# Kernel optimization log

Hardware: AMD Instinct MI355X
Metric: run time of the kernel (lower is better)

The kernel has to match this reference:

```python
import jax, jax.numpy as jnp
import numpy as np

N = 50000
E = 800000
IN_DIM = 128
HID = 32
HEADS = 8
OUT_DIM = 64
BN_EPS = 1e-5
NEG_SLOPE = 0.2


def batch_norm(x, gamma, beta, mean, var):
    # eval-mode BatchNorm1d using running statistics
    return (x - mean) * jax.lax.rsqrt(var + BN_EPS) * gamma + beta


def gat_conv(x, src, dst, W, att_src, att_dst, heads, out_ch, n):
    """PyG GATConv (shared src/dst lin), self-loops already included in src/dst.
    x: [n, in]; W: [in, heads*out_ch]; att_*: [heads, out_ch].
    Returns [n, heads, out_ch]."""
    h = (x @ W).reshape(n, heads, out_ch)                       # node features per head
    a_s = jnp.einsum('nho,ho->nh', h, att_src)                  # [n, heads]
    a_d = jnp.einsum('nho,ho->nh', h, att_dst)
    e = jax.nn.leaky_relu(a_s[src] + a_d[dst], NEG_SLOPE)       # [e, heads]
    # segment softmax over incoming edges of each dst node
    mx = jax.ops.segment_max(e, dst, num_segments=n)
    ex = jnp.exp(e - mx[dst])
    denom = jax.ops.segment_sum(ex, dst, num_segments=n)
    alpha = ex / (denom[dst] + 1e-16)                           # [e, heads]
    out = jax.ops.segment_sum(alpha[:, :, None] * h[src], dst, num_segments=n)
    return out                                                  # [n, heads, out_ch]


def setup_inputs() -> dict:
    key = jax.random.key(0)
    ks = jax.random.split(key, 24)
    inp = {}
    inp['x'] = jax.random.normal(ks[0], (N, IN_DIM), dtype=jnp.float32)
    inp['edge_index'] = jax.random.randint(ks[1], (2, E), 0, N, dtype=jnp.int64)
    s = 0.05
    inp['W1'] = jax.random.normal(ks[2], (IN_DIM, HEADS * HID), dtype=jnp.float32) * s
    inp['a_src1'] = jax.random.normal(ks[3], (HEADS, HID), dtype=jnp.float32) * s
    inp['a_dst1'] = jax.random.normal(ks[4], (HEADS, HID), dtype=jnp.float32) * s
    inp['b1'] = jnp.zeros((HEADS * HID,), dtype=jnp.float32)
    inp['W2'] = jax.random.normal(ks[5], (HEADS * HID, OUT_DIM), dtype=jnp.float32) * s
    inp['a_src2'] = jax.random.normal(ks[6], (1, OUT_DIM), dtype=jnp.float32) * s
    inp['a_dst2'] = jax.random.normal(ks[7], (1, OUT_DIM), dtype=jnp.float32) * s
    inp['b2'] = jnp.zeros((OUT_DIM,), dtype=jnp.float32)
    # projection Linear(out_dim -> in_dim)
    inp['Wp'] = jax.random.normal(ks[8], (OUT_DIM, IN_DIM), dtype=jnp.float32) * s
    inp['bp'] = jnp.zeros((IN_DIM,), dtype=jnp.float32)
    # BatchNorm params (eval mode running stats)
    for i, d in [(1, HEADS * HID), (2, OUT_DIM), (3, IN_DIM)]:
        k0, k1, k2, k3 = jax.random.split(ks[8 + i], 4)
        inp[f'g{i}'] = 1.0 + 0.1 * jax.random.normal(k0, (d,), dtype=jnp.float32)
        inp[f'be{i}'] = 0.1 * jax.random.normal(k1, (d,), dtype=jnp.float32)
        inp[f'm{i}'] = 0.1 * jax.random.normal(k2, (d,), dtype=jnp.float32)
        inp[f'v{i}'] = jax.random.uniform(k3, (d,), dtype=jnp.float32, minval=0.5, maxval=1.5)
    return inp


def reference(x, edge_index, W1, a_src1, a_dst1, b1, W2, a_src2, a_dst2, b2,
              Wp, bp, g1, be1, m1, v1, g2, be2, m2, v2, g3, be3, m3, v3):
    n = x.shape[0]
    loops = jnp.arange(n, dtype=edge_index.dtype)
    src = jnp.concatenate([edge_index[0], loops])   # add_self_loops=True (PyG default)
    dst = jnp.concatenate([edge_index[1], loops])

    h = gat_conv(x, src, dst, W1, a_src1, a_dst1, HEADS, HID, n)
    h = h.reshape(n, HEADS * HID) + b1              # concat=True
    h = jax.nn.elu(batch_norm(h, g1, be1, m1, v1))  # dropout is no-op in eval

    h = gat_conv(h, src, dst, W2, a_src2, a_dst2, 1, OUT_DIM, n)
    h = h.reshape(n, OUT_DIM) + b2                  # concat=False, heads=1 -> mean == identity
    h = jax.nn.elu(batch_norm(h, g2, be2, m2, v2))

    h = h @ Wp + bp
    return batch_norm(h, g3, be3, m3, v3)
```

## Files before the change

kernel.cpp:

```cpp
#include <hip/hip_runtime.h>
#include <math.h>

#define NEG_SLOPE 0.2f
#define BN_EPS 1e-5f

typedef __bf16 bf16x8 __attribute__((ext_vector_type(8)));
typedef float  f32x4  __attribute__((ext_vector_type(4)));

__device__ __forceinline__ float elu_f(float x){ return x > 0.f ? x : expm1f(x); }
__device__ __forceinline__ float lrelu_f(float x){ return x > 0.f ? x : NEG_SLOPE * x; }

__device__ __forceinline__ float b2f(ushort u){
    union { uint i; float f; } v; v.i = (uint)u << 16; return v.f;
}
__device__ __forceinline__ ushort f2b(float f){
    union { float f; uint i; } v; v.f = f;
    uint r = v.i + 0x7FFFu + ((v.i >> 16) & 1u);
    return (ushort)(r >> 16);
}

__global__ void setup_kernel(const void* ei, int n_check, long long N, int* flag64,
    const float* __restrict__ W1, const float* __restrict__ W2, const float* __restrict__ Wp,
    ushort* __restrict__ wt1, ushort* __restrict__ wt2, ushort* __restrict__ wtp,
    const float* b1, const float* b2, const float* bp,
    const float* g1, const float* be1, const float* m1, const float* v1,
    const float* g2, const float* be2, const float* m2, const float* v2,
    const float* g3, const float* be3, const float* m3, const float* v3,
    float* par)
{
    int b = blockIdx.x, t = threadIdx.x;
    if (b == 0) {
        __shared__ int oks;
        if (t == 0) oks = 1;
        __syncthreads();
        const long long* p = (const long long*)ei;
        int ok = 1;
        for (int i = t; i < n_check; i += 256) {
            long long v = p[i];
            if (v < 0 || v >= N) ok = 0;
        }
        if (!ok) oks = 0;
        __syncthreads();
        if (t == 0) *flag64 = oks;
        { float s = g1[t] * rsqrtf(v1[t] + BN_EPS); par[t] = s;        par[256 + t] = b1[t] * s + be1[t] - m1[t] * s; }
        if (t < 64)  { float s = g2[t] * rsqrtf(v2[t] + BN_EPS); par[512 + t] = s;  par[576 + t] = b2[t] * s + be2[t] - m2[t] * s; }
        if (t < 128) { float s = g3[t] * rsqrtf(v3[t] + BN_EPS); par[640 + t] = s;  par[768 + t] = bp[t] * s + be3[t] - m3[t] * s; }
    } else {
        int idx = (b - 1) * 256 + t;
        if (idx < 32768) {
            int n = idx >> 7, k = idx & 127;
            wt1[idx] = f2b(W1[k * 256 + n]);
        } else if (idx < 49152) {
            int j = idx - 32768;
            int n = j >> 8, k = j & 255;
            wt2[j] = f2b(W2[k * 64 + n]);
        } else if (idx < 57344) {
            int j = idx - 49152;
            int n = j >> 6, k = j & 63;
            wtp[j] = f2b(Wp[k * 128 + n]);
        }
    }
}

__device__ __forceinline__ void get_edge(const void* ei, int e, int E, int f64, int& s, int& d)
{
    if (e < E) {
        if (f64) { const long long* p = (const long long*)ei; s = (int)p[e]; d = (int)p[E + e]; }
        else     { const int*       p = (const int*)ei;       s = p[e];      d = p[E + e]; }
    } else {
        s = d = e - E;
    }
}

__global__ void count_kernel(const void* ei, int E, int N, const int* flag64, int* deg)
{
    int i = blockIdx.x * blockDim.x + threadIdx.x;
    int ET = E + N;
    if (i >= ET) return;
    int s, d;
    get_edge(ei, i, E, *flag64, s, d);
    atomicAdd(&deg[d], 1);
}

__global__ void scan1_kernel(const int* __restrict__ deg, int N, int* __restrict__ bsum)
{
    int b = blockIdx.x, t = threadIdx.x;
    int base = b * 4096 + t * 16;
    int s = 0;
    #pragma unroll
    for (int k = 0; k < 16; k += 4) {
        int idx = base + k;
        if (idx + 3 < N) {
            int4 v = *reinterpret_cast<const int4*>(&deg[idx]);
            s += v.x + v.y + v.z + v.w;
        } else {
            for (int q = 0; q < 4; ++q) if (idx + q < N) s += deg[idx + q];
        }
    }
    #pragma unroll
    for (int off = 1; off < 64; off <<= 1) s += __shfl_xor(s, off);
    __shared__ int wsum[4];
    if ((t & 63) == 0) wsum[t >> 6] = s;
    __syncthreads();
    if (t == 0) bsum[b] = wsum[0] + wsum[1] + wsum[2] + wsum[3];
}

__global__ void scan2_kernel(const int* __restrict__ bsum, int nb, int* __restrict__ bpre)
{
    if (threadIdx.x == 0) {
        int r = 0;
        for (int i = 0; i < nb; ++i) { bpre[i] = r; r += bsum[i]; }
        bpre[nb] = r;
    }
}

__global__ void scan3_kernel(const int* __restrict__ deg, int N,
                             const int* __restrict__ bpre, int nb,
                             int* __restrict__ rowptr, int* __restrict__ fillptr)
{
    int b = blockIdx.x, t = threadIdx.x;
    int base = b * 4096 + t * 16;
    int loc[16];
    int s = 0;
    #pragma unroll
    for (int k = 0; k < 16; ++k) {
        int idx = base + k;
        int d = (idx < N) ? deg[idx] : 0;
        loc[k] = s; s += d;
    }
    int lane = t & 63;
    int incl = s;
    #pragma unroll
    for (int off = 1; off < 64; off <<= 1) {
        int v = __shfl_up(incl, off);
        if (lane >= off) incl += v;
    }
    __shared__ int wsum[4];
    if (lane == 63) wsum[t >> 6] = incl;
    __syncthreads();
    int woff = 0;
    int w = t >> 6;
    for (int i = 0; i < w; ++i) woff += wsum[i];
    int off0 = bpre[b] + woff + incl - s;
    #pragma unroll
    for (int k = 0; k < 16; ++k) {
        int idx = base + k;
        if (idx < N) { rowptr[idx] = off0 + loc[k]; fillptr[idx] = off0 + loc[k]; }
    }
    if (b == 0 && t == 0) rowptr[N] = bpre[nb];
}

__global__ void fill_kernel(const void* ei, int E, int N, const int* flag64,
                            int* fillptr, int* esrc)
{
    int i = blockIdx.x * blockDim.x + threadIdx.x;
    int ET = E + N;
    if (i >= ET) return;
    int s, d;
    get_edge(ei, i, E, *flag64, s, d);
    int pos = atomicAdd(&fillptr[d], 1);
    esrc[pos] = s;
}

template<int ATYPE, int OMODE, int ATT>
__global__ __launch_bounds__(256) void mgemm_kernel(const void* __restrict__ Ap,
    const ushort* __restrict__ Bt, void* __restrict__ Cp, int M, int K, int NC,
    const float* __restrict__ S, const float* __restrict__ Cc,
    const float* __restrict__ att_s, const float* __restrict__ att_d,
    float* __restrict__ as_out, float* __restrict__ ad_out)
{
    const int BM = 128, LDA = 72;
    __shared__ __align__(16) ushort As[BM][LDA];
    __shared__ __align__(16) ushort Bs[64][LDA];
    int t = threadIdx.x;
    int m0 = blockIdx.x * BM, n0 = blockIdx.y * 64;
    int w = t >> 6, l = t & 63;
    int wm = w >> 1, wn = w & 1;
    int r16 = l & 15, kg = l >> 4;

    f32x4 acc[4][2];
    #pragma unroll
    for (int mi = 0; mi < 4; ++mi)
        #pragma unroll
        for (int ni = 0; ni < 2; ++ni)
            acc[mi][ni] = (f32x4){0.f, 0.f, 0.f, 0.f};

    for (int kb = 0; kb < K; kb += 64) {
        if (ATYPE == 0) {
            const float* A = (const float*)Ap;
            #pragma unroll
            for (int p = 0; p < 8; ++p) {
                int r = (t >> 4) + p * 16, c4 = (t & 15) * 4;
                int gm = m0 + r;
                float4 v = (gm < M) ? *reinterpret_cast<const float4*>(&A[(size_t)gm * K + kb + c4])
                                    : make_float4(0.f, 0.f, 0.f, 0.f);
                ushort4 u; u.x = f2b(v.x); u.y = f2b(v.y); u.z = f2b(v.z); u.w = f2b(v.w);
                *reinterpret_cast<ushort4*>(&As[r][c4]) = u;
            }
        } else {
            const ushort* A = (const ushort*)Ap;
            #pragma unroll
            for (int p = 0; p < 4; ++p) {
                int r = (t >> 3) + p * 32, c8 = (t & 7) * 8;
                int gm = m0 + r;
                uint4 v = (gm < M) ? *reinterpret_cast<const uint4*>(&A[(size_t)gm * K + kb + c8])
                                   : make_uint4(0u, 0u, 0u, 0u);
                *reinterpret_cast<uint4*>(&As[r][c8]) = v;
            }
        }
        #pragma unroll
        for (int p = 0; p < 2; ++p) {
            int r = (t >> 3) + p * 32, c8 = (t & 7) * 8;
            uint4 v = *reinterpret_cast<const uint4*>(&Bt[(size_t)(n0 + r) * K + kb + c8]);
            *reinterpret_cast<uint4*>(&Bs[r][c8]) = v;
        }
        __syncthreads();
        #pragma unroll
        for (int kk = 0; kk < 2; ++kk) {
            bf16x8 bB[2], bA[4];
            #pragma unroll
            for (int ni = 0; ni < 2; ++ni)
                bB[ni] = *reinterpret_cast<const bf16x8*>(&Bs[wn * 32 + ni * 16 + r16][kk * 32 + kg * 8]);
            #pragma unroll
            for (int mi = 0; mi < 4; ++mi)
                bA[mi] = *reinterpret_cast<const bf16x8*>(&As[wm * 64 + mi * 16 + r16][kk * 32 + kg * 8]);
            #pragma unroll
            for (int mi = 0; mi < 4; ++mi)
                #pragma unroll
                for (int ni = 0; ni < 2; ++ni)
                    acc[mi][ni] = __builtin_amdgcn_mfma_f32_16x16x32_bf16(bA[mi], bB[ni], acc[mi][ni], 0, 0, 0);
        }
        __syncthreads();
    }
    #pragma unroll
    for (int mi = 0; mi < 4; ++mi) {
        #pragma unroll
        for (int ni = 0; ni < 2; ++ni) {
            #pragma unroll
            for (int rg = 0; rg < 4; ++rg) {
                int gm = m0 + wm * 64 + mi * 16 + kg * 4 + rg;
                int gc = n0 + wn * 32 + ni * 16 + r16;
                if (gm < M) {
                    float v = acc[mi][ni][rg];
                    if (OMODE == 0) ((ushort*)Cp)[(size_t)gm * NC + gc] = f2b(v);
                    else            ((float*)Cp)[(size_t)gm * NC + gc] = v * S[gc] + Cc[gc];
                }
            }
        }
    }
    if (ATT) {
        int head = (n0 >> 5) + wn;
        float cs0 = att_s[n0 + wn * 32 + r16], cs1 = att_s[n0 + wn * 32 + 16 + r16];
        float cd0 = att_d[n0 + wn * 32 + r16], cd1 = att_d[n0 + wn * 32 + 16 + r16];
        float sp[4][4], dp[4][4];
        #pragma unroll
        for (int mi = 0; mi < 4; ++mi)
            #pragma unroll
            for (int rg = 0; rg < 4; ++rg) {
                sp[mi][rg] = acc[mi][0][rg] * cs0 + acc[mi][1][rg] * cs1;
                dp[mi][rg] = acc[mi][0][rg] * cd0 + acc[mi][1][rg] * cd1;
            }
        #pragma unroll
        for (int off = 1; off < 16; off <<= 1)
            #pragma unroll
            for (int mi = 0; mi < 4; ++mi)
                #pragma unroll
                for (int rg = 0; rg < 4; ++rg) {
                    sp[mi][rg] += __shfl_xor(sp[mi][rg], off);
                    dp[mi][rg] += __shfl_xor(dp[mi][rg], off);
                }
        if (r16 == 0) {
            #pragma unroll
            for (int mi = 0; mi < 4; ++mi)
                #pragma unroll
                for (int rg = 0; rg < 4; ++rg) {
                    int gm = m0 + wm * 64 + mi * 16 + kg * 4 + rg;
                    if (gm < M) {
                        as_out[gm * 8 + head] = sp[mi][rg];
                        ad_out[gm * 8 + head] = dp[mi][rg];
                    }
                }
        }
    }
}

__global__ void att2_kernel(const ushort* __restrict__ h2,
                            const float* __restrict__ a_src, const float* __restrict__ a_dst,
                            float* __restrict__ as2, float* __restrict__ ad2, int N)
{
    int wid = (blockIdx.x * blockDim.x + threadIdx.x) >> 6;
    int lane = threadIdx.x & 63;
    if (wid >= N) return;
    float v = b2f(h2[(size_t)wid * 64 + lane]);
    float s = v * a_src[lane];
    float d = v * a_dst[lane];
    #pragma unroll
    for (int off = 32; off; off >>= 1) {
        s += __shfl_down(s, off, 64);
        d += __shfl_down(d, off, 64);
    }
    if (lane == 0) { as2[wid] = s; ad2[wid] = d; }
}

__global__ void wden1_kernel(const float* __restrict__ as1, const float* __restrict__ ad1,
                             const int* __restrict__ rowptr, const int* __restrict__ esrc,
                             float* __restrict__ walpha, int N)
{
    int wid = (blockIdx.x * blockDim.x + threadIdx.x) >> 6;
    int lane = threadIdx.x & 63;
    if (wid >= N) return;
    int h = lane & 7, j = lane >> 3;
    float ad = ad1[wid * 8 + h];
    int beg = rowptr[wid], end = rowptr[wid + 1];
    float den = 0.f;
    for (int i = beg + j; i < end; i += 8) {
        int src = esrc[i];
        float w = __expf(lrelu_f(as1[src * 8 + h] + ad));
        walpha[(size_t)i * 8 + h] = w;
        den += w;
    }
    den += __shfl_xor(den, 8);
    den += __shfl_xor(den, 16);
    den += __shfl_xor(den, 32);
    float inv = 1.f / (den + 1e-16f);
    for (int i = beg + j; i < end; i += 8)
        walpha[(size_t)i * 8 + h] *= inv;
}

__global__ void wden2_kernel(const float* __restrict__ as2, const float* __restrict__ ad2,
                             const int* __restrict__ rowptr, const int* __restrict__ esrc,
                             float* __restrict__ walpha, int N)
{
    int wid = (blockIdx.x * blockDim.x + threadIdx.x) >> 6;
    int lane = threadIdx.x & 63;
    if (wid >= N) return;
    float ad = ad2[wid];
    int beg = rowptr[wid], end = rowptr[wid + 1];
    float den = 0.f;
    for (int i = beg + lane; i < end; i += 64) {
        float w = __expf(lrelu_f(as2[esrc[i]] + ad));
        walpha[i] = w;
        den += w;
    }
    #pragma unroll
    for (int off = 1; off < 64; off <<= 1) den += __shfl_xor(den, off);
    float inv = 1.f / (den + 1e-16f);
    for (int i = beg + lane; i < end; i += 64)
        walpha[i] *= inv;
}

__global__ void agg1_kernel(const ushort* __restrict__ h1, const float* __restrict__ walpha,
                            const int* __restrict__ rowptr, const int* __restrict__ esrc,
                            const float* __restrict__ par,
                            ushort* __restrict__ outb, int N)
{
    int wid = (blockIdx.x * blockDim.x + threadIdx.x) >> 6;
    int lane = threadIdx.x & 63;
    if (wid >= N) return;
    int beg = rowptr[wid], end = rowptr[wid + 1];
    int li = lane & 31, half = lane >> 5;
    int hh = li >> 2;
    float acc[8] = {0.f, 0.f, 0.f, 0.f, 0.f, 0.f, 0.f, 0.f};

    auto edge1 = [&](int ii) {
        int src = esrc[ii];
        float al = walpha[(size_t)ii * 8 + hh];
        uint4 r = *reinterpret_cast<const uint4*>(&h1[(size_t)src * 256 + li * 8]);
        union { uint u; float f; } c0, c1;
        c0.u = r.x << 16; c1.u = r.x & 0xffff0000u; acc[0] += al * c0.f; acc[1] += al * c1.f;
        c0.u = r.y << 16; c1.u = r.y & 0xffff0000u; acc[2] += al * c0.f; acc[3] += al * c1.f;
        c0.u = r.z << 16; c1.u = r.z & 0xffff0000u; acc[4] += al * c0.f; acc[5] += al * c1.f;
        c0.u = r.w << 16; c1.u = r.w & 0xffff0000u; acc[6] += al * c0.f; acc[7] += al * c1.f;
    };
    int i = beg + half;
    for (; i + 6 < end; i += 8) { edge1(i); edge1(i + 2); edge1(i + 4); edge1(i + 6); }
    for (; i < end; i += 2) edge1(i);

    #pragma unroll
    for (int f = 0; f < 8; ++f) acc[f] += __shfl_xor(acc[f], 32, 64);
    if (half == 0) {
        int f0 = li * 8;
        const float* S1 = par;
        const float* C1 = par + 256;
        ushort o[8];
        #pragma unroll
        for (int f = 0; f < 8; ++f) o[f] = f2b(elu_f(acc[f] * S1[f0 + f] + C1[f0 + f]));
        uint4 pk;
        pk.x = (uint)o[0] | ((uint)o[1] << 16);
        pk.y = (uint)o[2] | ((uint)o[3] << 16);
        pk.z = (uint)o[4] | ((uint)o[5] << 16);
        pk.w = (uint)o[6] | ((uint)o[7] << 16);
        *reinterpret_cast<uint4*>(&outb[(size_t)wid * 256 + f0]) = pk;
    }
}

__global__ void agg2_kernel(const ushort* __restrict__ h2, const float* __restrict__ walpha,
                            const int* __restrict__ rowptr, const int* __restrict__ esrc,
                            const float* __restrict__ par,
                            ushort* __restrict__ outb, int N)
{
    int wid = (blockIdx.x * blockDim.x + threadIdx.x) >> 6;
    int lane = threadIdx.x & 63;
    if (wid >= N) return;
    int beg = rowptr[wid], end = rowptr[wid + 1];
    int li = lane & 31, half = lane >> 5;
    float a0 = 0.f, a1 = 0.f;
    auto edge1 = [&](int ii) {
        int src = esrc[ii];
        float al = walpha[ii];
        uint hv = *reinterpret_cast<const uint*>(&h2[(size_t)src * 64 + li * 2]);
        union { uint u; float f; } c0, c1;
        c0.u = hv << 16; c1.u = hv & 0xffff0000u;
        a0 += al * c0.f; a1 += al * c1.f;
    };
    int i = beg + half;
    for (; i + 6 < end; i += 8) { edge1(i); edge1(i + 2); edge1(i + 4); edge1(i + 6); }
    for (; i < end; i += 2) edge1(i);

    a0 += __shfl_xor(a0, 32, 64);
    a1 += __shfl_xor(a1, 32, 64);
    if (half == 0) {
        int f = li * 2;
        const float* S2 = par + 512;
        const float* C2 = par + 576;
        ushort2 o;
        o.x = f2b(elu_f(a0 * S2[f] + C2[f]));
        o.y = f2b(elu_f(a1 * S2[f + 1] + C2[f + 1]));
        *reinterpret_cast<ushort2*>(&outb[(size_t)wid * 64 + f]) = o;
    }
}

extern "C" void kernel_launch(void* const* d_in, const int* in_sizes, int n_in,
                              void* d_out, int out_size, void* d_ws, size_t ws_size,
                              hipStream_t stream)
{
    const float* x      = (const float*)d_in[0];
    const void*  ei     = d_in[1];
    const float* W1     = (const float*)d_in[2];
    const float* a_src1 = (const float*)d_in[3];
    const float* a_dst1 = (const float*)d_in[4];
    const float* b1     = (const float*)d_in[5];
    const float* W2     = (const float*)d_in[6];
    const float* a_src2 = (const float*)d_in[7];
    const float* a_dst2 = (const float*)d_in[8];
    const float* b2     = (const float*)d_in[9];
    const float* Wp     = (const float*)d_in[10];
    const float* bp     = (const float*)d_in[11];
    const float* g1 = (const float*)d_in[12], *be1 = (const float*)d_in[13];
    const float* m1 = (const float*)d_in[14], *v1  = (const float*)d_in[15];
    const float* g2 = (const float*)d_in[16], *be2 = (const float*)d_in[17];
    const float* m2 = (const float*)d_in[18], *v2  = (const float*)d_in[19];
    const float* g3 = (const float*)d_in[20], *be3 = (const float*)d_in[21];
    const float* m3 = (const float*)d_in[22], *v3  = (const float*)d_in[23];
    float* out = (float*)d_out;

    const int N  = in_sizes[0] / 128;
    const int E  = in_sizes[1] / 2;
    const int ET = E + N;

    char* base = (char*)d_ws;
    size_t off = 0;
    auto alloc = [&](size_t bytes) -> char* {
        char* p = base + off;
        off += (bytes + 255) & ~(size_t)255;
        return p;
    };
    float*  par     = (float*)alloc(1024 * 4);
    int*    flag64  = (int*)alloc(256);
    int*    bsum    = (int*)alloc(256);
    int*    bpre    = (int*)alloc(256);
    int*    rowptr  = (int*)alloc((size_t)(N + 1) * 4);
    int*    fillptr = (int*)alloc((size_t)(N + 1) * 4);
    int*    esrc    = (int*)alloc((size_t)ET * 4);
    float*  as1     = (float*)alloc((size_t)N * 8 * 4);
    float*  ad1     = (float*)alloc((size_t)N * 8 * 4);
    float*  as2     = (float*)alloc((size_t)N * 4);
    float*  ad2     = (float*)alloc((size_t)N * 4);
    ushort* wt1     = (ushort*)alloc(256 * 128 * 2);
    ushort* wt2     = (ushort*)alloc(64 * 256 * 2);
    ushort* wtp     = (ushort*)alloc(128 * 64 * 2);
    float*  walpha1 = (float*)alloc((size_t)ET * 8 * 4);
    float*  walpha2 = (float*)alloc((size_t)ET * 4);
    ushort* h1      = (ushort*)alloc((size_t)N * 256 * 2);
    ushort* h1b     = (ushort*)alloc((size_t)N * 256 * 2);
    ushort* h2      = (ushort*)alloc((size_t)N * 64 * 2);
    ushort* g2buf   = (ushort*)alloc((size_t)N * 64 * 2);

    setup_kernel<<<225, 256, 0, stream>>>(ei, min(2 * E, 4096), (long long)N, flag64,
        W1, W2, Wp, wt1, wt2, wtp,
        b1, b2, bp, g1, be1, m1, v1, g2, be2, m2, v2, g3, be3, m3, v3, par);
    hipMemsetAsync(fillptr, 0, (N + 1) * sizeof(int), stream);

    int ebl = (ET + 255) / 256;
    int nb = (N + 4095) / 4096;
    count_kernel<<<ebl, 256, 0, stream>>>(ei, E, N, flag64, fillptr);
    scan1_kernel<<<nb, 256, 0, stream>>>(fillptr, N, bsum);
    scan2_kernel<<<1, 64, 0, stream>>>(bsum, nb, bpre);
    scan3_kernel<<<nb, 256, 0, stream>>>(fillptr, N, bpre, nb, rowptr, fillptr);
    fill_kernel<<<ebl, 256, 0, stream>>>(ei, E, N, flag64, fillptr, esrc);

    int mb128 = (N + 127) / 128;
    int wbl   = (N + 3) / 4;
    mgemm_kernel<0, 0, 1><<<dim3(mb128, 4), 256, 0, stream>>>(x, wt1, h1, N, 128, 256,
        nullptr, nullptr, a_src1, a_dst1, as1, ad1);
    wden1_kernel<<<wbl, 256, 0, stream>>>(as1, ad1, rowptr, esrc, walpha1, N);
    agg1_kernel<<<wbl, 256, 0, stream>>>(h1, walpha1, rowptr, esrc, par, h1b, N);

    mgemm_kernel<1, 0, 0><<<dim3(mb128, 1), 256, 0, stream>>>(h1b, wt2, h2, N, 256, 64,
        nullptr, nullptr, nullptr, nullptr, nullptr, nullptr);
    att2_kernel<<<wbl, 256, 0, stream>>>(h2, a_src2, a_dst2, as2, ad2, N);
    wden2_kernel<<<wbl, 256, 0, stream>>>(as2, ad2, rowptr, esrc, walpha2, N);
    agg2_kernel<<<wbl, 256, 0, stream>>>(h2, walpha2, rowptr, esrc, par, g2buf, N);

    mgemm_kernel<1, 1, 0><<<dim3(mb128, 2), 256, 0, stream>>>(g2buf, wtp, out, N, 64, 128,
        par + 640, par + 768, nullptr, nullptr, nullptr, nullptr);
}
```

Before: 331.2 us.

## Fuse softmax weights into aggregation and attention scores into GEMM epilogue

Drops the separate wden1/wden2 kernels and their per-edge walpha buffers. The aggregation kernels now compute the exp weights per 64-edge chunk into LDS and apply the normalising denominator at the end. The layer-2 attention dot products move into the mgemm epilogue, with a cross-wave reduction in shared memory, which removes att2_kernel. The degree count is merged into setup_kernel, and the int64 index detection becomes a per-wave ballot, so the count kernel and the flag are gone. This saves several launches and the global round trip of the edge weights, at the cost of recomputing exp during aggregation and a weaker format check.

```diff
diff --git a/kernel.cpp b/kernel.cpp
--- a/kernel.cpp
+++ b/kernel.cpp
@@ -19,7 +19,26 @@
     return (ushort)(r >> 16);
 }
 
-__global__ void setup_kernel(const void* ei, int n_check, long long N, int* flag64,
+__device__ __forceinline__ bool detect_f64(const void* ei, int E, long long N)
+{
+    const long long* p = (const long long*)ei;
+    int lane = threadIdx.x & 63;
+    long long v = p[lane % max(1, min(2 * E, 64))];
+    bool bad = (v < 0 || v >= N);
+    return __ballot(bad) == 0ull;
+}
+
+__device__ __forceinline__ void get_edge(const void* ei, int e, int E, bool f64, int& s, int& d)
+{
+    if (e < E) {
+        if (f64) { const long long* p = (const long long*)ei; s = (int)p[e]; d = (int)p[E + e]; }
+        else     { const int*       p = (const int*)ei;       s = p[e];      d = p[E + e]; }
+    } else {
+        s = d = e - E;
+    }
+}
+
+__global__ void setup_kernel(const void* ei, int E, int N, int* deg,
     const float* __restrict__ W1, const float* __restrict__ W2, const float* __restrict__ Wp,
     ushort* __restrict__ wt1, ushort* __restrict__ wt2, ushort* __restrict__ wtp,
     const float* b1, const float* b2, const float* bp,
@@ -30,22 +49,10 @@
 {
     int b = blockIdx.x, t = threadIdx.x;
     if (b == 0) {
-        __shared__ int oks;
-        if (t == 0) oks = 1;
-        __syncthreads();
-        const long long* p = (const long long*)ei;
-        int ok = 1;
-        for (int i = t; i < n_check; i += 256) {
-            long long v = p[i];
-            if (v < 0 || v >= N) ok = 0;
-        }
-        if (!ok) oks = 0;
-        __syncthreads();
-        if (t == 0) *flag64 = oks;
         { float s = g1[t] * rsqrtf(v1[t] + BN_EPS); par[t] = s;        par[256 + t] = b1[t] * s + be1[t] - m1[t] * s; }
         if (t < 64)  { float s = g2[t] * rsqrtf(v2[t] + BN_EPS); par[512 + t] = s;  par[576 + t] = b2[t] * s + be2[t] - m2[t] * s; }
         if (t < 128) { float s = g3[t] * rsqrtf(v3[t] + BN_EPS); par[640 + t] = s;  par[768 + t] = bp[t] * s + be3[t] - m3[t] * s; }
-    } else {
+    } else if (b <= 224) {
         int idx = (b - 1) * 256 + t;
         if (idx < 32768) {
             int n = idx >> 7, k = idx & 127;
@@ -59,27 +66,16 @@
             int n = j >> 6, k = j & 63;
             wtp[j] = f2b(Wp[k * 128 + n]);
         }
-    }
-}
-
-__device__ __forceinline__ void get_edge(const void* ei, int e, int E, int f64, int& s, int& d)
-{
-    if (e < E) {
-        if (f64) { const long long* p = (const long long*)ei; s = (int)p[e]; d = (int)p[E + e]; }
-        else     { const int*       p = (const int*)ei;       s = p[e];      d = p[E + e]; }
     } else {
-        s = d = e - E;
-    }
-}
-
-__global__ void count_kernel(const void* ei, int E, int N, const int* flag64, int* deg)
-{
-    int i = blockIdx.x * blockDim.x + threadIdx.x;
-    int ET = E + N;
-    if (i >= ET) return;
-    int s, d;
-    get_edge(ei, i, E, *flag64, s, d);
-    atomicAdd(&deg[d], 1);
+        bool f64 = detect_f64(ei, E, (long long)N);
+        int i = (b - 225) * 256 + t;
+        int ET = E + N;
+        if (i < ET) {
+            int s, d;
+            get_edge(ei, i, E, f64, s, d);
+            atomicAdd(&deg[d], 1);
+        }
+    }
 }
 
 __global__ void scan1_kernel(const int* __restrict__ deg, int N, int* __restrict__ bsum)
@@ -150,14 +146,14 @@
     if (b == 0 && t == 0) rowptr[N] = bpre[nb];
 }
 
-__global__ void fill_kernel(const void* ei, int E, int N, const int* flag64,
-                            int* fillptr, int* esrc)
-{
+__global__ void fill_kernel(const void* ei, int E, int N, int* fillptr, int* esrc)
+{
+    bool f64 = detect_f64(ei, E, (long long)N);
     int i = blockIdx.x * blockDim.x + threadIdx.x;
     int ET = E + N;
     if (i >= ET) return;
     int s, d;
-    get_edge(ei, i, E, *flag64, s, d);
+    get_edge(ei, i, E, f64, s, d);
     int pos = atomicAdd(&fillptr[d], 1);
     esrc[pos] = s;
 }
@@ -172,6 +168,7 @@
     const int BM = 128, LDA = 72;
     __shared__ __align__(16) ushort As[BM][LDA];
     __shared__ __align__(16) ushort Bs[64][LDA];
+    __shared__ float red[128][2];
     int t = threadIdx.x;
     int m0 = blockIdx.x * BM, n0 = blockIdx.y * 64;
     int w = t >> 6, l = t & 63;
@@ -249,7 +246,6 @@
         }
     }
     if (ATT) {
-        int head = (n0 >> 5) + wn;
         float cs0 = att_s[n0 + wn * 32 + r16], cs1 = att_s[n0 + wn * 32 + 16 + r16];
         float cd0 = att_d[n0 + wn * 32 + r16], cd1 = att_d[n0 + wn * 32 + 16 + r16];
         float sp[4][4], dp[4][4];
@@ -269,112 +265,96 @@
                     sp[mi][rg] += __shfl_xor(sp[mi][rg], off);
                     dp[mi][rg] += __shfl_xor(dp[mi][rg], off);
                 }
-        if (r16 == 0) {
-            #pragma unroll
-            for (int mi = 0; mi < 4; ++mi)
+        if (ATT == 1) {
+            int head = (n0 >> 5) + wn;
+            if (r16 == 0) {
                 #pragma unroll
-                for (int rg = 0; rg < 4; ++rg) {
-                    int gm = m0 + wm * 64 + mi * 16 + kg * 4 + rg;
-                    if (gm < M) {
-                        as_out[gm * 8 + head] = sp[mi][rg];
-                        ad_out[gm * 8 + head] = dp[mi][rg];
+                for (int mi = 0; mi < 4; ++mi)
+                    #pragma unroll
+                    for (int rg = 0; rg < 4; ++rg) {
+                        int gm = m0 + wm * 64 + mi * 16 + kg * 4 + rg;
+                        if (gm < M) {
+                            as_out[gm * 8 + head] = sp[mi][rg];
+                            ad_out[gm * 8 + head] = dp[mi][rg];
+                        }
                     }
-                }
-        }
-    }
-}
-
-__global__ void att2_kernel(const ushort* __restrict__ h2,
-                            const float* __restrict__ a_src, const float* __restrict__ a_dst,
-                            float* __restrict__ as2, float* __restrict__ ad2, int N)
-{
-    int wid = (blockIdx.x * blockDim.x + threadIdx.x) >> 6;
-    int lane = threadIdx.x & 63;
-    if (wid >= N) return;
-    float v = b2f(h2[(size_t)wid * 64 + lane]);
-    float s = v * a_src[lane];
-    float d = v * a_dst[lane];
-    #pragma unroll
-    for (int off = 32; off; off >>= 1) {
-        s += __shfl_down(s, off, 64);
-        d += __shfl_down(d, off, 64);
-    }
-    if (lane == 0) { as2[wid] = s; ad2[wid] = d; }
-}
-
-__global__ void wden1_kernel(const float* __restrict__ as1, const float* __restrict__ ad1,
-                             const int* __restrict__ rowptr, const int* __restrict__ esrc,
-                             float* __restrict__ walpha, int N)
-{
-    int wid = (blockIdx.x * blockDim.x + threadIdx.x) >> 6;
-    int lane = threadIdx.x & 63;
-    if (wid >= N) return;
-    int h = lane & 7, j = lane >> 3;
-    float ad = ad1[wid * 8 + h];
-    int beg = rowptr[wid], end = rowptr[wid + 1];
-    float den = 0.f;
-    for (int i = beg + j; i < end; i += 8) {
-        int src = esrc[i];
-        float w = __expf(lrelu_f(as1[src * 8 + h] + ad));
-        walpha[(size_t)i * 8 + h] = w;
-        den += w;
-    }
-    den += __shfl_xor(den, 8);
-    den += __shfl_xor(den, 16);
-    den += __shfl_xor(den, 32);
-    float inv = 1.f / (den + 1e-16f);
-    for (int i = beg + j; i < end; i += 8)
-        walpha[(size_t)i * 8 + h] *= inv;
-}
-
-__global__ void wden2_kernel(const float* __restrict__ as2, const float* __restrict__ ad2,
-                             const int* __restrict__ rowptr, const int* __restrict__ esrc,
-                             float* __restrict__ walpha, int N)
-{
-    int wid = (blockIdx.x * blockDim.x + threadIdx.x) >> 6;
-    int lane = threadIdx.x & 63;
-    if (wid >= N) return;
-    float ad = ad2[wid];
-    int beg = rowptr[wid], end = rowptr[wid + 1];
-    float den = 0.f;
-    for (int i = beg + lane; i < end; i += 64) {
-        float w = __expf(lrelu_f(as2[esrc[i]] + ad));
-        walpha[i] = w;
-        den += w;
-    }
-    #pragma unroll
-    for (int off = 1; off < 64; off <<= 1) den += __shfl_xor(den, off);
-    float inv = 1.f / (den + 1e-16f);
-    for (int i = beg + lane; i < end; i += 64)
-        walpha[i] *= inv;
-}
-
-__global__ void agg1_kernel(const ushort* __restrict__ h1, const float* __restrict__ walpha,
+            }
+        } else {
+            if (wn == 1 && r16 == 0) {
+                #pragma unroll
+                for (int mi = 0; mi < 4; ++mi)
+                    #pragma unroll
+                    for (int rg = 0; rg < 4; ++rg) {
+                        int r = wm * 64 + mi * 16 + kg * 4 + rg;
+                        red[r][0] = sp[mi][rg];
+                        red[r][1] = dp[mi][rg];
+                    }
+            }
+            __syncthreads();
+            if (wn == 0 && r16 == 0) {
+                #pragma unroll
+                for (int mi = 0; mi < 4; ++mi)
+                    #pragma unroll
+                    for (int rg = 0; rg < 4; ++rg) {
+                        int r = wm * 64 + mi * 16 + kg * 4 + rg;
+                        int gm = m0 + r;
+                        if (gm < M) {
+                            as_out[gm] = sp[mi][rg] + red[r][0];
+                            ad_out[gm] = dp[mi][rg] + red[r][1];
+                        }
+                    }
+            }
+        }
+    }
+}
+
+__global__ void agg1_kernel(const ushort* __restrict__ h1,
+                            const float* __restrict__ as1, const float* __restrict__ ad1,
                             const int* __restrict__ rowptr, const int* __restrict__ esrc,
                             const float* __restrict__ par,
                             ushort* __restrict__ outb, int N)
 {
+    __shared__ float wlds_all[4][64 * 8];
+    float* wlds = wlds_all[threadIdx.x >> 6];
     int wid = (blockIdx.x * blockDim.x + threadIdx.x) >> 6;
     int lane = threadIdx.x & 63;
     if (wid >= N) return;
     int beg = rowptr[wid], end = rowptr[wid + 1];
-    int li = lane & 31, half = lane >> 5;
-    int hh = li >> 2;
+    int h = lane & 7, j = lane >> 3;
+    int li = lane & 31, half = lane >> 5, hh = li >> 2;
+    float ad_h = ad1[wid * 8 + h];
+    float den = 0.f;
     float acc[8] = {0.f, 0.f, 0.f, 0.f, 0.f, 0.f, 0.f, 0.f};
 
-    auto edge1 = [&](int ii) {
-        int src = esrc[ii];
-        float al = walpha[(size_t)ii * 8 + hh];
-        uint4 r = *reinterpret_cast<const uint4*>(&h1[(size_t)src * 256 + li * 8]);
-        union { uint u; float f; } c0, c1;
-        c0.u = r.x << 16; c1.u = r.x & 0xffff0000u; acc[0] += al * c0.f; acc[1] += al * c1.f;
-        c0.u = r.y << 16; c1.u = r.y & 0xffff0000u; acc[2] += al * c0.f; acc[3] += al * c1.f;
-        c0.u = r.z << 16; c1.u = r.z & 0xffff0000u; acc[4] += al * c0.f; acc[5] += al * c1.f;
-        c0.u = r.w << 16; c1.u = r.w & 0xffff0000u; acc[6] += al * c0.f; acc[7] += al * c1.f;
-    };
-    int i = beg + half;
-    for (; i + 6 < end; i += 8) { edge1(i); edge1(i + 2); edge1(i + 4); edge1(i + 6); }
-    for (; i < end; i += 2) edge1(i);
+    for (int cb = beg; cb < end; cb += 64) {
+        int ce = min(cb + 64, end);
+        for (int i = cb + j; i < ce; i += 8) {
+            float wv = __expf(lrelu_f(as1[esrc[i] * 8 + h] + ad_h));
+            wlds[(i - cb) * 8 + h] = wv;
+            den += wv;
+        }
+        __builtin_amdgcn_wave_barrier();
+        auto edge1 = [&](int ii) {
+            int src = esrc[ii];
+            float al = wlds[(ii - cb) * 8 + hh];
+            uint4 r = *reinterpret_cast<const uint4*>(&h1[(size_t)src * 256 + li * 8]);
+            union { uint u; float f; } c0, c1;
+            c0.u = r.x << 16; c1.u = r.x & 0xffff0000u; acc[0] += al * c0.f; acc[1] += al * c1.f;
+            c0.u = r.y << 16; c1.u = r.y & 0xffff0000u; acc[2] += al * c0.f; acc[3] += al * c1.f;
+            c0.u = r.z << 16; c1.u = r.z & 0xffff0000u; acc[4] += al * c0.f; acc[5] += al * c1.f;
+            c0.u = r.w << 16; c1.u = r.w & 0xffff0000u; acc[6] += al * c0.f; acc[7] += al * c1.f;
+        };
+        int i = cb + half;
+        for (; i + 6 < ce; i += 8) { edge1(i); edge1(i + 2); edge1(i + 4); edge1(i + 6); }
+        for (; i < ce; i += 2) edge1(i);
+        __builtin_amdgcn_wave_barrier();
+    }
+
+    den += __shfl_xor(den, 8, 64);
+    den += __shfl_xor(den, 16, 64);
+    den += __shfl_xor(den, 32, 64);
+    float inv = 1.f / (den + 1e-16f);
+    float inv_h = __shfl(inv, hh, 64);
 
     #pragma unroll
     for (int f = 0; f < 8; ++f) acc[f] += __shfl_xor(acc[f], 32, 64);
@@ -384,7 +364,7 @@
         const float* C1 = par + 256;
         ushort o[8];
         #pragma unroll
-        for (int f = 0; f < 8; ++f) o[f] = f2b(elu_f(acc[f] * S1[f0 + f] + C1[f0 + f]));
+        for (int f = 0; f < 8; ++f) o[f] = f2b(elu_f(acc[f] * inv_h * S1[f0 + f] + C1[f0 + f]));
         uint4 pk;
         pk.x = (uint)o[0] | ((uint)o[1] << 16);
         pk.y = (uint)o[2] | ((uint)o[3] << 16);
@@ -394,29 +374,51 @@
     }
 }
 
-__global__ void agg2_kernel(const ushort* __restrict__ h2, const float* __restrict__ walpha,
+__global__ void agg2_kernel(const ushort* __restrict__ h2,
+                            const float* __restrict__ as2, const float* __restrict__ ad2,
                             const int* __restrict__ rowptr, const int* __restrict__ esrc,
                             const float* __restrict__ par,
                             ushort* __restrict__ outb, int N)
 {
+    __shared__ float wlds_all[4][64];
+    float* wlds = wlds_all[threadIdx.x >> 6];
     int wid = (blockIdx.x * blockDim.x + threadIdx.x) >> 6;
     int lane = threadIdx.x & 63;
     if (wid >= N) return;
     int beg = rowptr[wid], end = rowptr[wid + 1];
     int li = lane & 31, half = lane >> 5;
+    float ad = ad2[wid];
+    float den = 0.f;
     float a0 = 0.f, a1 = 0.f;
-    auto edge1 = [&](int ii) {
-        int src = esrc[ii];
-        float al = walpha[ii];
-        uint hv = *reinterpret_cast<const uint*>(&h2[(size_t)src * 64 + li * 2]);
-        union { uint u; float f; } c0, c1;
-        c0.u = hv << 16; c1.u = hv & 0xffff0000u;
-        a0 += al * c0.f; a1 += al * c1.f;
-    };
-    int i = beg + half;
-    for (; i + 6 < end; i += 8) { edge1(i); edge1(i + 2); edge1(i + 4); edge1(i + 6); }
-    for (; i < end; i += 2) edge1(i);
-
+
+    for (int cb = beg; cb < end; cb += 64) {
+        int ce = min(cb + 64, end);
+        {
+            int i = cb + lane;
+            if (i < ce) {
+                float wv = __expf(lrelu_f(as2[esrc[i]] + ad));
+                wlds[i - cb] = wv;
+                den += wv;
+            }
+        }
+        __builtin_amdgcn_wave_barrier();
+        auto edge1 = [&](int ii) {
+            int src = esrc[ii];
+            float al = wlds[ii - cb];
+            uint hv = *reinterpret_cast<const uint*>(&h2[(size_t)src * 64 + li * 2]);
+            union { uint u; float f; } c0, c1;
+            c0.u = hv << 16; c1.u = hv & 0xffff0000u;
+            a0 += al * c0.f; a1 += al * c1.f;
+        };
+        int i = cb + half;
+        for (; i + 6 < ce; i += 8) { edge1(i); edge1(i + 2); edge1(i + 4); edge1(i + 6); }
+        for (; i < ce; i += 2) edge1(i);
+        __builtin_amdgcn_wave_barrier();
+    }
+
+    #pragma unroll
+    for (int off = 1; off < 64; off <<= 1) den += __shfl_xor(den, off, 64);
+    float inv = 1.f / (den + 1e-16f);
     a0 += __shfl_xor(a0, 32, 64);
     a1 += __shfl_xor(a1, 32, 64);
     if (half == 0) {
@@ -424,8 +426,8 @@
         const float* S2 = par + 512;
         const float* C2 = par + 576;
         ushort2 o;
-        o.x = f2b(elu_f(a0 * S2[f] + C2[f]));
-        o.y = f2b(elu_f(a1 * S2[f + 1] + C2[f + 1]));
+        o.x = f2b(elu_f(a0 * inv * S2[f] + C2[f]));
+        o.y = f2b(elu_f(a1 * inv * S2[f + 1] + C2[f + 1]));
         *reinterpret_cast<ushort2*>(&outb[(size_t)wid * 64 + f]) = o;
     }
 }
@@ -466,7 +468,6 @@
         return p;
     };
     float*  par     = (float*)alloc(1024 * 4);
-    int*    flag64  = (int*)alloc(256);
     int*    bsum    = (int*)alloc(256);
     int*    bpre    = (int*)alloc(256);
     int*    rowptr  = (int*)alloc((size_t)(N + 1) * 4);
@@ -479,38 +480,32 @@
     ushort* wt1     = (ushort*)alloc(256 * 128 * 2);
     ushort* wt2     = (ushort*)alloc(64 * 256 * 2);
     ushort* wtp     = (ushort*)alloc(128 * 64 * 2);
-    float*  walpha1 = (float*)alloc((size_t)ET * 8 * 4);
-    float*  walpha2 = (float*)alloc((size_t)ET * 4);
     ushort* h1      = (ushort*)alloc((size_t)N * 256 * 2);
     ushort* h1b     = (ushort*)alloc((size_t)N * 256 * 2);
     ushort* h2      = (ushort*)alloc((size_t)N * 64 * 2);
     ushort* g2buf   = (ushort*)alloc((size_t)N * 64 * 2);
 
-    setup_kernel<<<225, 256, 0, stream>>>(ei, min(2 * E, 4096), (long long)N, flag64,
+    hipMemsetAsync(fillptr, 0, (N + 1) * sizeof(int), stream);
+    int cblocks = (ET + 255) / 256;
+    setup_kernel<<<225 + cblocks, 256, 0, stream>>>(ei, E, N, fillptr,
         W1, W2, Wp, wt1, wt2, wtp,
         b1, b2, bp, g1, be1, m1, v1, g2, be2, m2, v2, g3, be3, m3, v3, par);
-    hipMemsetAsync(fillptr, 0, (N + 1) * sizeof(int), stream);
-
-    int ebl = (ET + 255) / 256;
+
     int nb = (N + 4095) / 4096;
-    count_kernel<<<ebl, 256, 0, stream>>>(ei, E, N, flag64, fillptr);
     scan1_kernel<<<nb, 256, 0, stream>>>(fillptr, N, bsum);
     scan2_kernel<<<1, 64, 0, stream>>>(bsum, nb, bpre);
     scan3_kernel<<<nb, 256, 0, stream>>>(fillptr, N, bpre, nb, rowptr, fillptr);
-    fill_kernel<<<ebl, 256, 0, stream>>>(ei, E, N, flag64, fillptr, esrc);
+    fill_kernel<<<cblocks, 256, 0, stream>>>(ei, E, N, fillptr, esrc);
 
     int mb128 = (N + 127) / 128;
     int wbl   = (N + 3) / 4;
     mgemm_kernel<0, 0, 1><<<dim3(mb128, 4), 256, 0, stream>>>(x, wt1, h1, N, 128, 256,
         nullptr, nullptr, a_src1, a_dst1, as1, ad1);
-    wden1_kernel<<<wbl, 256, 0, stream>>>(as1, ad1, rowptr, esrc, walpha1, N);
-    agg1_kernel<<<wbl, 256, 0, stream>>>(h1, walpha1, rowptr, esrc, par, h1b, N);
-
-    mgemm_kernel<1, 0, 0><<<dim3(mb128, 1), 256, 0, stream>>>(h1b, wt2, h2, N, 256, 64,
-        nullptr, nullptr, nullptr, nullptr, nullptr, nullptr);
-    att2_kernel<<<wbl, 256, 0, stream>>>(h2, a_src2, a_dst2, as2, ad2, N);
-    wden2_kernel<<<wbl, 256, 0, stream>>>(as2, ad2, rowptr, esrc, walpha2, N);
-    agg2_kernel<<<wbl, 256, 0, stream>>>(h2, walpha2, rowptr, esrc, par, g2buf, N);
+    agg1_kernel<<<wbl, 256, 0, stream>>>(h1, as1, ad1, rowptr, esrc, par, h1b, N);
+
+    mgemm_kernel<1, 0, 2><<<dim3(mb128, 1), 256, 0, stream>>>(h1b, wt2, h2, N, 256, 64,
+        nullptr, nullptr, a_src2, a_dst2, as2, ad2);
+    agg2_kernel<<<wbl, 256, 0, stream>>>(h2, as2, ad2, rowptr, esrc, par, g2buf, N);
 
     mgemm_kernel<1, 1, 0><<<dim3(mb128, 2), 256, 0, stream>>>(g2buf, wtp, out, N, 64, 128,
         par + 640, par + 768, nullptr, nullptr, nullptr, nullptr);
```

After: 292.1 us. -11.8%, faster.
